# Kernel tuning notes

Hardware: AMD Instinct MI355X
Metric: run time of the kernel (lower is better)

The kernel has to match this reference:

```python
import jax, jax.numpy as jnp
import numpy as np

N_NODES = 100000
N_EDGES = 1600000
N_GRAPHS = 128
DIM = 128
N_LAYERS = 4
EPS = 1e-5


def setup_inputs() -> dict:
    key = jax.random.key(0)
    ks = jax.random.split(key, 8)
    h = jax.random.normal(ks[0], (N_NODES, DIM), dtype=jnp.float32)
    src = jax.random.randint(ks[1], (N_EDGES,), 0, N_NODES, dtype=jnp.int32)
    dst = jax.random.randint(ks[2], (N_EDGES,), 0, N_NODES, dtype=jnp.int32)
    graph_id = jnp.sort(jax.random.randint(ks[3], (N_NODES,), 0, N_GRAPHS, dtype=jnp.int32))
    sc = 1.0 / np.sqrt(DIM)
    W_embed = jax.random.normal(ks[4], (DIM, DIM), dtype=jnp.float32) * sc
    b_embed = jnp.zeros((DIM,), jnp.float32)
    W_layers = jax.random.normal(ks[5], (N_LAYERS, DIM, DIM), dtype=jnp.float32) * sc
    b_layers = jnp.zeros((N_LAYERS, DIM), jnp.float32)
    gamma = jnp.ones((N_LAYERS, DIM), jnp.float32)
    beta = jnp.zeros((N_LAYERS, DIM), jnp.float32)
    return {"h": h, "src": src, "dst": dst, "graph_id": graph_id,
            "W_embed": W_embed, "b_embed": b_embed, "W_layers": W_layers,
            "b_layers": b_layers, "gamma": gamma, "beta": beta}


def _gcn_forward(h, src, dst, graph_id, W_embed, b_embed, W_layers, b_layers, gamma, beta):
    # symmetric GraphConv normalization (norm='both'): D_out^{-1/2} on src, D_in^{-1/2} on dst
    ones_e = jnp.ones((src.shape[0],), h.dtype)
    deg_out = jax.ops.segment_sum(ones_e, src, num_segments=N_NODES)
    deg_in = jax.ops.segment_sum(ones_e, dst, num_segments=N_NODES)
    norm_src = jax.lax.rsqrt(jnp.maximum(deg_out, 1.0))
    norm_dst = jax.lax.rsqrt(jnp.maximum(deg_in, 1.0))

    # input embedding (dropout = identity in eval)
    h = h @ W_embed + b_embed

    for l in range(N_LAYERS):
        h_in = h
        # gather-aggregate-scatter: m_e = h_src * norm_src; sum into dst; scale by norm_dst
        m = (h * norm_src[:, None])[src]                         # [E, D]
        agg = jax.ops.segment_sum(m, dst, num_segments=N_NODES)  # [N, D]
        hl = (agg * norm_dst[:, None]) @ W_layers[l] + b_layers[l]
        # batch norm over node dimension (training-mode batch stats)
        mu = jnp.mean(hl, axis=0)
        var = jnp.var(hl, axis=0)
        hl = (hl - mu) * jax.lax.rsqrt(var + EPS) * gamma[l] + beta[l]
        hl = jax.nn.relu(hl)
        h = hl + h_in  # residual (dims match all layers)

    # mean readout per graph
    sums = jax.ops.segment_sum(h, graph_id, num_segments=N_GRAPHS)           # [G, D]
    cnts = jax.ops.segment_sum(jnp.ones((N_NODES,), h.dtype), graph_id, num_segments=N_GRAPHS)
    return sums / jnp.maximum(cnts, 1.0)[:, None]


def reference(h, src, dst, graph_id, W_embed, b_embed, W_layers, b_layers, gamma, beta):
    return _gcn_forward(h, src, dst, graph_id, W_embed, b_embed, W_layers, b_layers, gamma, beta)
```

## Files before the change

kernel.cpp:

```cpp
#include <hip/hip_runtime.h>
#include <hip/hip_bf16.h>
#include <hip/hip_fp16.h>


#define N_NODES 100000
#define N_EDGES 1600000
#define N_GRAPHS 128
#define DIM 128
#define N_LAYERS 4
#define BN_EPS 1e-5f
#define NBUCK 196
#define EPB 6250
#define SREP 64

typedef __attribute__((ext_vector_type(8))) _Float16 half8;
typedef __attribute__((ext_vector_type(4))) float floatx4;
typedef __attribute__((ext_vector_type(2))) float floatx2;

__global__ __launch_bounds__(256) void binA_k(const int* __restrict__ src,
                                              const int* __restrict__ dst,
                                              int* __restrict__ cnt_d,
                                              int* __restrict__ cnt_s) {
  __shared__ int hd[NBUCK], hs[NBUCK];
  int t = threadIdx.x;
  for (int i = t; i < NBUCK; i += 256) { hd[i] = 0; hs[i] = 0; }
  __syncthreads();
  int e0 = blockIdx.x * EPB;
  for (int e = e0 + t; e < e0 + EPB; e += 256) {
    atomicAdd(&hd[dst[e] >> 9], 1);
    atomicAdd(&hs[src[e] >> 9], 1);
  }
  __syncthreads();
  for (int i = t; i < NBUCK; i += 256) {
    if (hd[i]) atomicAdd(&cnt_d[i], hd[i]);
    if (hs[i]) atomicAdd(&cnt_s[i], hs[i]);
  }
}

__global__ __launch_bounds__(256) void scan196_k(
    const int* __restrict__ cnt_d, const int* __restrict__ cnt_s,
    int* __restrict__ base_d, int* __restrict__ cur_d,
    int* __restrict__ base_s, int* __restrict__ cur_s,
    int* __restrict__ row_start) {
  __shared__ int sd[256], ss[256];
  int t = threadIdx.x;
  int vd = (t < NBUCK) ? cnt_d[t] : 0;
  int vs = (t < NBUCK) ? cnt_s[t] : 0;
  sd[t] = vd;
  ss[t] = vs;
  __syncthreads();
  for (int off = 1; off < 256; off <<= 1) {
    int ad = (t >= off) ? sd[t - off] : 0;
    int as = (t >= off) ? ss[t - off] : 0;
    __syncthreads();
    sd[t] += ad;
    ss[t] += as;
    __syncthreads();
  }
  if (t < NBUCK) {
    base_d[t] = sd[t] - vd;
    cur_d[t] = sd[t] - vd;
    base_s[t] = ss[t] - vs;
    cur_s[t] = ss[t] - vs;
  }
  if (t == 0) {
    base_d[NBUCK] = N_EDGES;
    base_s[NBUCK] = N_EDGES;
    row_start[N_NODES] = N_EDGES;
  }
}

__global__ __launch_bounds__(256) void scat_k(
    const int* __restrict__ src, const int* __restrict__ dst,
    int* __restrict__ cur_d, int* __restrict__ cur_s,
    int* __restrict__ packed, unsigned short* __restrict__ locs) {
  __shared__ int hd[NBUCK], hs[NBUCK];
  int t = threadIdx.x;
  for (int i = t; i < NBUCK; i += 256) { hd[i] = 0; hs[i] = 0; }
  __syncthreads();
  int e0 = blockIdx.x * EPB;
  for (int e = e0 + t; e < e0 + EPB; e += 256) {
    atomicAdd(&hd[dst[e] >> 9], 1);
    atomicAdd(&hs[src[e] >> 9], 1);
  }
  __syncthreads();
  if (t < NBUCK) {
    hd[t] = atomicAdd(&cur_d[t], hd[t]);
    hs[t] = atomicAdd(&cur_s[t], hs[t]);
  }
  __syncthreads();
  for (int e = e0 + t; e < e0 + EPB; e += 256) {
    int s = src[e], d = dst[e];
    int slot = atomicAdd(&hd[d >> 9], 1);
    packed[slot] = ((d & 511) << 17) | s;
    int slot2 = atomicAdd(&hs[s >> 9], 1);
    locs[slot2] = (unsigned short)(s & 511);
  }
}

__global__ __launch_bounds__(256) void cd_k(const int* __restrict__ base_d,
                                            const int* __restrict__ packed,
                                            int* __restrict__ row_start,
                                            int* __restrict__ csr_src) {
  __shared__ int sdeg[512], sinc[512], scur[512];
  int t = threadIdx.x;
  int b = blockIdx.x;
  int nbase = b << 9;
  int e0 = base_d[b], e1 = base_d[b + 1];
  sdeg[t] = 0;
  sdeg[t + 256] = 0;
  __syncthreads();
  for (int e = e0 + t; e < e1; e += 256) atomicAdd(&sdeg[packed[e] >> 17], 1);
  __syncthreads();
  sinc[t] = sdeg[t];
  sinc[t + 256] = sdeg[t + 256];
  __syncthreads();
  for (int off = 1; off < 512; off <<= 1) {
    int a0 = (t >= off) ? sinc[t - off] : 0;
    int i1 = t + 256;
    int a1 = (i1 >= off) ? sinc[i1 - off] : 0;
    __syncthreads();
    sinc[t] += a0;
    sinc[i1] += a1;
    __syncthreads();
  }
#pragma unroll
  for (int half = 0; half < 2; ++half) {
    int j = t + half * 256;
    int lofs = e0 + sinc[j] - sdeg[j];
    scur[j] = lofs;
    int node = nbase + j;
    if (node < N_NODES) row_start[node] = lofs;
  }
  __syncthreads();
  for (int e = e0 + t; e < e1; e += 256) {
    int p = packed[e];
    int slot = atomicAdd(&scur[p >> 17], 1);
    csr_src[slot] = p & 0x1FFFF;
  }
}

__global__ __launch_bounds__(256) void cs_k(const int* __restrict__ base_s,
                                            const unsigned short* __restrict__ locs,
                                            int* __restrict__ deg_out) {
  __shared__ int sdeg[512];
  int t = threadIdx.x;
  int b = blockIdx.x;
  int nbase = b << 9;
  int e0 = base_s[b], e1 = base_s[b + 1];
  sdeg[t] = 0;
  sdeg[t + 256] = 0;
  __syncthreads();
  for (int e = e0 + t; e < e1; e += 256) atomicAdd(&sdeg[locs[e]], 1);
  __syncthreads();
#pragma unroll
  for (int half = 0; half < 2; ++half) {
    int j = t + half * 256;
    int node = nbase + j;
    if (node < N_NODES) deg_out[node] = sdeg[j];
  }
}

__global__ __launch_bounds__(256) void norm_k(const int* __restrict__ deg_out,
                                              const int* __restrict__ row_start,
                                              float* __restrict__ norm_src,
                                              float* __restrict__ norm_dst) {
  int i = blockIdx.x * 256 + threadIdx.x;
  if (i < N_NODES) {
    int din = row_start[i + 1] - row_start[i];
    int dso = deg_out[i] > 1 ? deg_out[i] : 1;
    int dsi = din > 1 ? din : 1;
    norm_src[i] = rsqrtf((float)dso);
    norm_dst[i] = rsqrtf((float)dsi);
  }
}

__global__ __launch_bounds__(256) void wswz_k(const float* __restrict__ W,
                                              __half* __restrict__ Bsw) {
  int w = blockIdx.x >> 3, ct = blockIdx.x & 7;
  int ks = threadIdx.x >> 6, lane = threadIdx.x & 63;
  int n = ct * 16 + (lane & 15);
  int k0 = ks * 32 + (lane >> 4) * 8;
  const float* Wm = W + (size_t)w * 16384;
  __half* o = Bsw + ((((size_t)w * 8 + ct) * 4 + ks) * 64 + lane) * 8;
#pragma unroll
  for (int j = 0; j < 8; ++j) o[j] = __float2half(Wm[(k0 + j) * 128 + n]);
}

__device__ inline void mfma_core16(const __half* sA,
                                   const __half* __restrict__ Bsw,
                                   floatx4 (&acc)[8], int w, int lane,
                                   int quad, int lrow) {
#pragma unroll
  for (int ct = 0; ct < 8; ++ct) acc[ct] = (floatx4)(0.f);
#pragma unroll
  for (int ks = 0; ks < 4; ++ks) {
    int m = w * 16 + lrow;
    half8 afrag = *(const half8*)(&sA[m * 136 + ks * 32 + quad * 8]);
#pragma unroll
    for (int ct = 0; ct < 8; ++ct) {
      half8 bfrag = *(const half8*)(&Bsw[(((size_t)ct * 4 + ks) * 64 + lane) * 8]);
      acc[ct] = __builtin_amdgcn_mfma_f32_16x16x32_f16(afrag, bfrag, acc[ct],
                                                       0, 0, 0);
    }
  }
}

__global__ __launch_bounds__(256) void mfma_gemm_f32in(
    const float* __restrict__ X32, const __half* __restrict__ Bsw,
    const float* __restrict__ bias, __half* __restrict__ A16,
    unsigned char* __restrict__ S8, const float* __restrict__ norm_src) {
  __shared__ __half sA[64 * 136];
  const int tid = threadIdx.x;
  const int w = tid >> 6, lane = tid & 63;
  const int quad = lane >> 4, lrow = lane & 15;
  const int row_base = blockIdx.x * 64;

#pragma unroll
  for (int i = 0; i < 8; ++i) {
    int g = i * 256 + tid;
    int r = g >> 5, q = g & 31;
    int row = row_base + r;
    float4 v = make_float4(0.f, 0.f, 0.f, 0.f);
    if (row < N_NODES) v = ((const float4*)X32)[(size_t)row * 32 + q];
    union { __half2 h[2]; float f[2]; } u;
    u.h[0] = __floats2half2_rn(v.x, v.y);
    u.h[1] = __floats2half2_rn(v.z, v.w);
    *(float2*)(&sA[r * 136 + q * 4]) = *(float2*)u.f;
  }
  __syncthreads();

  floatx4 acc[8];
  mfma_core16(sA, Bsw, acc, w, lane, quad, lrow);

#pragma unroll
  for (int ct = 0; ct < 8; ++ct) {
    int col = ct * 16 + lrow;
    float b = bias[col];
#pragma unroll
    for (int reg = 0; reg < 4; ++reg) {
      int row = row_base + w * 16 + quad * 4 + reg;
      if (row < N_NODES) {
        float y = acc[ct][reg] + b;
        A16[(size_t)row * 128 + col] = __float2half(y);
        unsigned pb =
            __builtin_amdgcn_cvt_pk_fp8_f32(y * norm_src[row], 0.f, 0, false);
        S8[(size_t)row * 128 + col] = (unsigned char)(pb & 0xFF);
      }
    }
  }
}

__global__ __launch_bounds__(256) void mfma_gemm_f16(
    const __half* __restrict__ X16, const __half* __restrict__ Bsw,
    const float* __restrict__ bias, __half* __restrict__ hl16,
    float* __restrict__ stats) {
  __shared__ __half sA[64 * 136];
  const int tid = threadIdx.x;
  const int w = tid >> 6, lane = tid & 63;
  const int quad = lane >> 4, lrow = lane & 15;
  const int row_base = blockIdx.x * 64;

#pragma unroll
  for (int i = 0; i < 4; ++i) {
    int g = i * 256 + tid;
    int r = g >> 4, p = g & 15;
    int row = row_base + r;
    float4 v = make_float4(0.f, 0.f, 0.f, 0.f);
    if (row < N_NODES) v = ((const float4*)X16)[(size_t)row * 16 + p];
    *(float4*)(&sA[r * 136 + p * 8]) = v;
  }
  __syncthreads();

  floatx4 acc[8];
  mfma_core16(sA, Bsw, acc, w, lane, quad, lrow);

  float psum[8], pqsum[8];
#pragma unroll
  for (int ct = 0; ct < 8; ++ct) {
    int col = ct * 16 + lrow;
    float b = bias[col];
    psum[ct] = 0.f;
    pqsum[ct] = 0.f;
#pragma unroll
    for (int reg = 0; reg < 4; ++reg) {
      int row = row_base + w * 16 + quad * 4 + reg;
      if (row < N_NODES) {
        float y = acc[ct][reg] + b;
        hl16[(size_t)row * 128 + col] = __float2half(y);
        psum[ct] += y;
        pqsum[ct] += y * y;
      }
    }
  }

#pragma unroll
  for (int ct = 0; ct < 8; ++ct) {
    psum[ct] += __shfl_xor(psum[ct], 16, 64);
    psum[ct] += __shfl_xor(psum[ct], 32, 64);
    pqsum[ct] += __shfl_xor(pqsum[ct], 16, 64);
    pqsum[ct] += __shfl_xor(pqsum[ct], 32, 64);
  }
  __syncthreads();
  float* sred = (float*)sA;
  if (quad == 0) {
#pragma unroll
    for (int ct = 0; ct < 8; ++ct) {
      sred[w * 128 + ct * 16 + lrow] = psum[ct];
      sred[512 + w * 128 + ct * 16 + lrow] = pqsum[ct];
    }
  }
  __syncthreads();
  if (tid < 128) {
    float s = sred[tid] + sred[128 + tid] + sred[256 + tid] + sred[384 + tid];
    float q = sred[512 + tid] + sred[640 + tid] + sred[768 + tid] +
              sred[896 + tid];
    float* st = stats + (size_t)(blockIdx.x & (SREP - 1)) * 256;
    atomicAdd(&st[tid], s);
    atomicAdd(&st[128 + tid], q);
  }
}

__global__ __launch_bounds__(128) void bn_fin_k(const float* __restrict__ stats,
                                                const float* __restrict__ gamma,
                                                const float* __restrict__ beta,
                                                float* __restrict__ sc_sh) {
  int c = threadIdx.x;
  float s = 0.f, q = 0.f;
  for (int r = 0; r < SREP; ++r) {
    s += stats[r * 256 + c];
    q += stats[r * 256 + 128 + c];
  }
  const float invn = 1.0f / (float)N_NODES;
  float mean = s * invn;
  float var = q * invn - mean * mean;
  var = fmaxf(var, 0.f);
  float sc = gamma[c] * rsqrtf(var + BN_EPS);
  sc_sh[c] = sc;
  sc_sh[128 + c] = beta[c] - mean * sc;
}

__global__ __launch_bounds__(256) void bnrelu_k(
    const __half* __restrict__ hl16, __half* __restrict__ A16,
    unsigned char* __restrict__ S8, const float* __restrict__ sc_sh,
    const float* __restrict__ norm_src, int write_scaled) {
  int idx = blockIdx.x * 256 + threadIdx.x;
  int node = idx >> 4;
  int c8 = idx & 15;
  float4 hv4 = *(const float4*)(hl16 + (size_t)idx * 8);
  float4 av4 = *(const float4*)(A16 + (size_t)idx * 8);
  const __half2* hp = (const __half2*)&hv4;
  const __half2* ap = (const __half2*)&av4;
  const float4* sv = (const float4*)sc_sh;
  float4 s0 = sv[c8 * 2], s1 = sv[c8 * 2 + 1];
  float4 b0 = sv[32 + c8 * 2], b1 = sv[32 + c8 * 2 + 1];
  float n = write_scaled ? norm_src[node] : 0.f;
  float2 f0 = __half22float2(hp[0]), f1 = __half22float2(hp[1]);
  float2 f2 = __half22float2(hp[2]), f3 = __half22float2(hp[3]);
  float2 a0 = __half22float2(ap[0]), a1 = __half22float2(ap[1]);
  float2 a2 = __half22float2(ap[2]), a3 = __half22float2(ap[3]);
  float v[8];
  v[0] = fmaxf(f0.x * s0.x + b0.x, 0.f) + a0.x;
  v[1] = fmaxf(f0.y * s0.y + b0.y, 0.f) + a0.y;
  v[2] = fmaxf(f1.x * s0.z + b0.z, 0.f) + a1.x;
  v[3] = fmaxf(f1.y * s0.w + b0.w, 0.f) + a1.y;
  v[4] = fmaxf(f2.x * s1.x + b1.x, 0.f) + a2.x;
  v[5] = fmaxf(f2.y * s1.y + b1.y, 0.f) + a2.y;
  v[6] = fmaxf(f3.x * s1.z + b1.z, 0.f) + a3.x;
  v[7] = fmaxf(f3.y * s1.w + b1.w, 0.f) + a3.y;
  union { __half2 h[4]; float4 f; } ua;
#pragma unroll
  for (int q = 0; q < 4; ++q)
    ua.h[q] = __floats2half2_rn(v[2 * q], v[2 * q + 1]);
  *(float4*)(A16 + (size_t)idx * 8) = ua.f;
  if (write_scaled) {
    unsigned lo = 0, hi = 0;
    lo = __builtin_amdgcn_cvt_pk_fp8_f32(v[0] * n, v[1] * n, lo, false);
    lo = __builtin_amdgcn_cvt_pk_fp8_f32(v[2] * n, v[3] * n, lo, true);
    hi = __builtin_amdgcn_cvt_pk_fp8_f32(v[4] * n, v[5] * n, hi, false);
    hi = __builtin_amdgcn_cvt_pk_fp8_f32(v[6] * n, v[7] * n, hi, true);
    ((uint2*)S8)[idx] = make_uint2(lo, hi);
  }
}

__device__ inline void accf8(float (&a)[8], uint2 v) {
  floatx2 f;
  f = __builtin_amdgcn_cvt_pk_f32_fp8(v.x, false); a[0] += f.x; a[1] += f.y;
  f = __builtin_amdgcn_cvt_pk_f32_fp8(v.x, true);  a[2] += f.x; a[3] += f.y;
  f = __builtin_amdgcn_cvt_pk_f32_fp8(v.y, false); a[4] += f.x; a[5] += f.y;
  f = __builtin_amdgcn_cvt_pk_f32_fp8(v.y, true);  a[6] += f.x; a[7] += f.y;
}

__global__ __launch_bounds__(256) void gather_k(
    const uint2* __restrict__ Hs, const int* __restrict__ row_start,
    const int* __restrict__ csr_src, const float* __restrict__ norm_dst,
    __half* __restrict__ out) {
  int node = (blockIdx.x * 256 + threadIdx.x) >> 4;
  int lane = threadIdx.x & 15;
  if (node >= N_NODES) return;
  int s0 = row_start[node], s1 = row_start[node + 1];
  float a[8] = {0.f, 0.f, 0.f, 0.f, 0.f, 0.f, 0.f, 0.f};
  for (int e = s0; e < s1; e += 16) {
    int cnt = s1 - e;
    if (cnt > 16) cnt = 16;
    int idx = (lane < cnt) ? csr_src[e + lane] : 0;
    int j = 0;
    for (; j + 8 <= cnt; j += 8) {
      uint2 v0 = Hs[(size_t)__shfl(idx, j, 16) * 16 + lane];
      uint2 v1 = Hs[(size_t)__shfl(idx, j + 1, 16) * 16 + lane];
      uint2 v2 = Hs[(size_t)__shfl(idx, j + 2, 16) * 16 + lane];
      uint2 v3 = Hs[(size_t)__shfl(idx, j + 3, 16) * 16 + lane];
      uint2 v4 = Hs[(size_t)__shfl(idx, j + 4, 16) * 16 + lane];
      uint2 v5 = Hs[(size_t)__shfl(idx, j + 5, 16) * 16 + lane];
      uint2 v6 = Hs[(size_t)__shfl(idx, j + 6, 16) * 16 + lane];
      uint2 v7 = Hs[(size_t)__shfl(idx, j + 7, 16) * 16 + lane];
      accf8(a, v0); accf8(a, v1); accf8(a, v2); accf8(a, v3);
      accf8(a, v4); accf8(a, v5); accf8(a, v6); accf8(a, v7);
    }
    for (; j + 4 <= cnt; j += 4) {
      uint2 v0 = Hs[(size_t)__shfl(idx, j, 16) * 16 + lane];
      uint2 v1 = Hs[(size_t)__shfl(idx, j + 1, 16) * 16 + lane];
      uint2 v2 = Hs[(size_t)__shfl(idx, j + 2, 16) * 16 + lane];
      uint2 v3 = Hs[(size_t)__shfl(idx, j + 3, 16) * 16 + lane];
      accf8(a, v0); accf8(a, v1); accf8(a, v2); accf8(a, v3);
    }
    for (; j < cnt; ++j) {
      accf8(a, Hs[(size_t)__shfl(idx, j, 16) * 16 + lane]);
    }
  }
  float nd = norm_dst[node];
  union { __half2 h[4]; float4 f; } u;
  u.h[0] = __floats2half2_rn(a[0] * nd, a[1] * nd);
  u.h[1] = __floats2half2_rn(a[2] * nd, a[3] * nd);
  u.h[2] = __floats2half2_rn(a[4] * nd, a[5] * nd);
  u.h[3] = __floats2half2_rn(a[6] * nd, a[7] * nd);
  ((float4*)(out + (size_t)node * 128))[lane] = u.f;
}

__global__ __launch_bounds__(256) void gbounds_k(const int* __restrict__ gid,
                                                 int* __restrict__ gstart) {
  int g = threadIdx.x;
  if (g > N_GRAPHS) return;
  int lo = 0, hi = N_NODES;
  while (lo < hi) {
    int mid = (lo + hi) >> 1;
    if (gid[mid] < g) lo = mid + 1; else hi = mid;
  }
  gstart[g] = lo;
}

__global__ __launch_bounds__(128) void gsum_k(const __half* __restrict__ A16,
                                              const int* __restrict__ gid,
                                              float* gsum) {
  int c = threadIdx.x;
  int n0 = blockIdx.x * 128;
  int n1 = n0 + 128;
  if (n1 > N_NODES) n1 = N_NODES;
  int cur = gid[n0];
  float local = 0.f;
  for (int n = n0; n < n1; ++n) {
    int g = gid[n];
    if (g != cur) {
      atomicAdd(&gsum[cur * 128 + c], local);
      local = 0.f;
      cur = g;
    }
    local += __half2float(A16[(size_t)n * 128 + c]);
  }
  atomicAdd(&gsum[cur * 128 + c], local);
}

__global__ __launch_bounds__(128) void gout_k(const float* __restrict__ gsum,
                                              const int* __restrict__ gstart,
                                              float* __restrict__ out) {
  int g = blockIdx.x, c = threadIdx.x;
  float cnt = (float)(gstart[g + 1] - gstart[g]);
  if (cnt < 1.f) cnt = 1.f;
  out[g * 128 + c] = gsum[g * 128 + c] / cnt;
}

extern "C" void kernel_launch(void* const* d_in, const int* in_sizes, int n_in,
                              void* d_out, int out_size, void* d_ws,
                              size_t ws_size, hipStream_t stream) {
  const float* h = (const float*)d_in[0];
  const int* src = (const int*)d_in[1];
  const int* dst = (const int*)d_in[2];
  const int* gid = (const int*)d_in[3];
  const float* W_embed = (const float*)d_in[4];
  const float* b_embed = (const float*)d_in[5];
  const float* W_layers = (const float*)d_in[6];
  const float* b_layers = (const float*)d_in[7];
  const float* gamma = (const float*)d_in[8];
  const float* beta = (const float*)d_in[9];
  float* out = (float*)d_out;
  (void)in_sizes; (void)n_in; (void)out_size; (void)ws_size;

  char* ws = (char*)d_ws;
  size_t o = 0;
  auto alloc = [&](size_t bytes) -> char* {
    char* p = ws + o;
    o = (o + bytes + 255) & ~(size_t)255;
    return p;
  };
  int* cnt_d = (int*)alloc(NBUCK * 4);
  int* cnt_s = (int*)alloc(NBUCK * 4);
  int* base_d = (int*)alloc((NBUCK + 1) * 4);
  int* cur_d = (int*)alloc(NBUCK * 4);
  int* base_s = (int*)alloc((NBUCK + 1) * 4);
  int* cur_s = (int*)alloc(NBUCK * 4);
  float* norm_src = (float*)alloc(N_NODES * 4);
  float* norm_dst = (float*)alloc(N_NODES * 4);
  int* deg_out = (int*)alloc(N_NODES * 4);
  int* row_start = (int*)alloc((N_NODES + 1) * 4);
  int* csr_src = (int*)alloc((size_t)N_EDGES * 4);
  int* packed = (int*)alloc((size_t)N_EDGES * 4);
  unsigned short* locs = (unsigned short*)alloc((size_t)N_EDGES * 2);
  float* stats = (float*)alloc((size_t)SREP * 256 * 4);
  float* gsum = (float*)alloc(N_GRAPHS * 128 * 4);
  int* gstart = (int*)alloc((N_GRAPHS + 1) * 4);
  float* sc_sh = (float*)alloc(256 * 4);
  __half* Bsw = (__half*)alloc(5 * 16384 * 2);
  __half* A16 = (__half*)alloc((size_t)N_NODES * 128 * 2);
  unsigned char* P0f8 = (unsigned char*)alloc((size_t)N_NODES * 128);
  __half* P1h = (__half*)alloc((size_t)N_NODES * 128 * 2);
  __half* H16 = (__half*)alloc((size_t)N_NODES * 128 * 2);

  hipMemsetAsync(cnt_d, 0, 2048, stream);
  hipMemsetAsync(stats, 0, SREP * 256 * 4 + 65536, stream);

  binA_k<<<256, 256, 0, stream>>>(src, dst, cnt_d, cnt_s);
  scan196_k<<<1, 256, 0, stream>>>(cnt_d, cnt_s, base_d, cur_d, base_s, cur_s,
                                   row_start);
  scat_k<<<256, 256, 0, stream>>>(src, dst, cur_d, cur_s, packed, locs);
  cd_k<<<NBUCK, 256, 0, stream>>>(base_d, packed, row_start, csr_src);
  cs_k<<<NBUCK, 256, 0, stream>>>(base_s, locs, deg_out);
  norm_k<<<(N_NODES + 255) / 256, 256, 0, stream>>>(deg_out, row_start,
                                                    norm_src, norm_dst);

  wswz_k<<<8, 256, 0, stream>>>(W_embed, Bsw);
  wswz_k<<<32, 256, 0, stream>>>(W_layers, Bsw + 16384);

  mfma_gemm_f32in<<<(N_NODES + 63) / 64, 256, 0, stream>>>(
      h, Bsw, b_embed, A16, P0f8, norm_src);

  for (int l = 0; l < N_LAYERS; ++l) {
    if (l) hipMemsetAsync(stats, 0, SREP * 256 * 4, stream);
    gather_k<<<(N_NODES * 16 + 255) / 256, 256, 0, stream>>>(
        (const uint2*)P0f8, row_start, csr_src, norm_dst, P1h);
    mfma_gemm_f16<<<(N_NODES + 63) / 64, 256, 0, stream>>>(
        P1h, Bsw + (size_t)(1 + l) * 16384, b_layers + l * DIM, H16, stats);
    bn_fin_k<<<1, 128, 0, stream>>>(stats, gamma + l * DIM, beta + l * DIM,
                                    sc_sh);
    bnrelu_k<<<(N_NODES * 16 + 255) / 256, 256, 0, stream>>>(
        H16, A16, P0f8, sc_sh, norm_src, (l < N_LAYERS - 1) ? 1 : 0);
  }

  gbounds_k<<<1, 256, 0, stream>>>(gid, gstart);
  gsum_k<<<(N_NODES + 127) / 128, 128, 0, stream>>>(A16, gid, gsum);
  gout_k<<<N_GRAPHS, 128, 0, stream>>>(gsum, gstart, out);
}
```

Baseline: 575.0 us.

## Widen gather loads, reuse block histograms, fold norm kernel, batch launches

```diff
diff --git a/kernel.cpp b/kernel.cpp
--- a/kernel.cpp
+++ b/kernel.cpp
@@ -20,7 +20,9 @@
 __global__ __launch_bounds__(256) void binA_k(const int* __restrict__ src,
                                               const int* __restrict__ dst,
                                               int* __restrict__ cnt_d,
-                                              int* __restrict__ cnt_s) {
+                                              int* __restrict__ cnt_s,
+                                              int* __restrict__ bh_d,
+                                              int* __restrict__ bh_s) {
   __shared__ int hd[NBUCK], hs[NBUCK];
   int t = threadIdx.x;
   for (int i = t; i < NBUCK; i += 256) { hd[i] = 0; hs[i] = 0; }
@@ -32,8 +34,11 @@
   }
   __syncthreads();
   for (int i = t; i < NBUCK; i += 256) {
-    if (hd[i]) atomicAdd(&cnt_d[i], hd[i]);
-    if (hs[i]) atomicAdd(&cnt_s[i], hs[i]);
+    int v = hd[i], v2 = hs[i];
+    bh_d[blockIdx.x * NBUCK + i] = v;
+    bh_s[blockIdx.x * NBUCK + i] = v2;
+    if (v) atomicAdd(&cnt_d[i], v);
+    if (v2) atomicAdd(&cnt_s[i], v2);
   }
 }
 
@@ -73,15 +78,13 @@
 __global__ __launch_bounds__(256) void scat_k(
     const int* __restrict__ src, const int* __restrict__ dst,
     int* __restrict__ cur_d, int* __restrict__ cur_s,
+    const int* __restrict__ bh_d, const int* __restrict__ bh_s,
     int* __restrict__ packed, unsigned short* __restrict__ locs) {
   __shared__ int hd[NBUCK], hs[NBUCK];
   int t = threadIdx.x;
-  for (int i = t; i < NBUCK; i += 256) { hd[i] = 0; hs[i] = 0; }
-  __syncthreads();
-  int e0 = blockIdx.x * EPB;
-  for (int e = e0 + t; e < e0 + EPB; e += 256) {
-    atomicAdd(&hd[dst[e] >> 9], 1);
-    atomicAdd(&hs[src[e] >> 9], 1);
+  for (int i = t; i < NBUCK; i += 256) {
+    hd[i] = bh_d[blockIdx.x * NBUCK + i];
+    hs[i] = bh_s[blockIdx.x * NBUCK + i];
   }
   __syncthreads();
   if (t < NBUCK) {
@@ -89,6 +92,7 @@
     hs[t] = atomicAdd(&cur_s[t], hs[t]);
   }
   __syncthreads();
+  int e0 = blockIdx.x * EPB;
   for (int e = e0 + t; e < e0 + EPB; e += 256) {
     int s = src[e], d = dst[e];
     int slot = atomicAdd(&hd[d >> 9], 1);
@@ -101,7 +105,8 @@
 __global__ __launch_bounds__(256) void cd_k(const int* __restrict__ base_d,
                                             const int* __restrict__ packed,
                                             int* __restrict__ row_start,
-                                            int* __restrict__ csr_src) {
+                                            int* __restrict__ csr_src,
+                                            float* __restrict__ norm_dst) {
   __shared__ int sdeg[512], sinc[512], scur[512];
   int t = threadIdx.x;
   int b = blockIdx.x;
@@ -130,7 +135,11 @@
     int lofs = e0 + sinc[j] - sdeg[j];
     scur[j] = lofs;
     int node = nbase + j;
-    if (node < N_NODES) row_start[node] = lofs;
+    if (node < N_NODES) {
+      row_start[node] = lofs;
+      int d = sdeg[j];
+      norm_dst[node] = rsqrtf((float)(d > 1 ? d : 1));
+    }
   }
   __syncthreads();
   for (int e = e0 + t; e < e1; e += 256) {
@@ -142,7 +151,7 @@
 
 __global__ __launch_bounds__(256) void cs_k(const int* __restrict__ base_s,
                                             const unsigned short* __restrict__ locs,
-                                            int* __restrict__ deg_out) {
+                                            float* __restrict__ norm_src) {
   __shared__ int sdeg[512];
   int t = threadIdx.x;
   int b = blockIdx.x;
@@ -157,32 +166,23 @@
   for (int half = 0; half < 2; ++half) {
     int j = t + half * 256;
     int node = nbase + j;
-    if (node < N_NODES) deg_out[node] = sdeg[j];
-  }
-}
-
-__global__ __launch_bounds__(256) void norm_k(const int* __restrict__ deg_out,
-                                              const int* __restrict__ row_start,
-                                              float* __restrict__ norm_src,
-                                              float* __restrict__ norm_dst) {
-  int i = blockIdx.x * 256 + threadIdx.x;
-  if (i < N_NODES) {
-    int din = row_start[i + 1] - row_start[i];
-    int dso = deg_out[i] > 1 ? deg_out[i] : 1;
-    int dsi = din > 1 ? din : 1;
-    norm_src[i] = rsqrtf((float)dso);
-    norm_dst[i] = rsqrtf((float)dsi);
-  }
-}
-
-__global__ __launch_bounds__(256) void wswz_k(const float* __restrict__ W,
+    if (node < N_NODES) {
+      int d = sdeg[j];
+      norm_src[node] = rsqrtf((float)(d > 1 ? d : 1));
+    }
+  }
+}
+
+__global__ __launch_bounds__(256) void wswz_k(const float* __restrict__ W_embed,
+                                              const float* __restrict__ W_layers,
                                               __half* __restrict__ Bsw) {
-  int w = blockIdx.x >> 3, ct = blockIdx.x & 7;
+  int m = blockIdx.x >> 3, ct = blockIdx.x & 7;
+  const float* Wm =
+      (m == 0) ? W_embed : (W_layers + (size_t)(m - 1) * 16384);
   int ks = threadIdx.x >> 6, lane = threadIdx.x & 63;
   int n = ct * 16 + (lane & 15);
   int k0 = ks * 32 + (lane >> 4) * 8;
-  const float* Wm = W + (size_t)w * 16384;
-  __half* o = Bsw + ((((size_t)w * 8 + ct) * 4 + ks) * 64 + lane) * 8;
+  __half* o = Bsw + ((((size_t)m * 8 + ct) * 4 + ks) * 64 + lane) * 8;
 #pragma unroll
   for (int j = 0; j < 8; ++j) o[j] = __float2half(Wm[(k0 + j) * 128 + n]);
 }
@@ -383,58 +383,53 @@
   }
 }
 
-__device__ inline void accf8(float (&a)[8], uint2 v) {
+__device__ inline void accf8x16(float (&a)[16], uint4 v) {
   floatx2 f;
-  f = __builtin_amdgcn_cvt_pk_f32_fp8(v.x, false); a[0] += f.x; a[1] += f.y;
-  f = __builtin_amdgcn_cvt_pk_f32_fp8(v.x, true);  a[2] += f.x; a[3] += f.y;
-  f = __builtin_amdgcn_cvt_pk_f32_fp8(v.y, false); a[4] += f.x; a[5] += f.y;
-  f = __builtin_amdgcn_cvt_pk_f32_fp8(v.y, true);  a[6] += f.x; a[7] += f.y;
+  f = __builtin_amdgcn_cvt_pk_f32_fp8(v.x, false); a[0] += f.x;  a[1] += f.y;
+  f = __builtin_amdgcn_cvt_pk_f32_fp8(v.x, true);  a[2] += f.x;  a[3] += f.y;
+  f = __builtin_amdgcn_cvt_pk_f32_fp8(v.y, false); a[4] += f.x;  a[5] += f.y;
+  f = __builtin_amdgcn_cvt_pk_f32_fp8(v.y, true);  a[6] += f.x;  a[7] += f.y;
+  f = __builtin_amdgcn_cvt_pk_f32_fp8(v.z, false); a[8] += f.x;  a[9] += f.y;
+  f = __builtin_amdgcn_cvt_pk_f32_fp8(v.z, true);  a[10] += f.x; a[11] += f.y;
+  f = __builtin_amdgcn_cvt_pk_f32_fp8(v.w, false); a[12] += f.x; a[13] += f.y;
+  f = __builtin_amdgcn_cvt_pk_f32_fp8(v.w, true);  a[14] += f.x; a[15] += f.y;
 }
 
 __global__ __launch_bounds__(256) void gather_k(
-    const uint2* __restrict__ Hs, const int* __restrict__ row_start,
+    const uint4* __restrict__ Hs, const int* __restrict__ row_start,
     const int* __restrict__ csr_src, const float* __restrict__ norm_dst,
     __half* __restrict__ out) {
-  int node = (blockIdx.x * 256 + threadIdx.x) >> 4;
-  int lane = threadIdx.x & 15;
+  int node = (blockIdx.x * 256 + threadIdx.x) >> 3;
+  int lane = threadIdx.x & 7;
   if (node >= N_NODES) return;
   int s0 = row_start[node], s1 = row_start[node + 1];
-  float a[8] = {0.f, 0.f, 0.f, 0.f, 0.f, 0.f, 0.f, 0.f};
-  for (int e = s0; e < s1; e += 16) {
+  float a[16];
+#pragma unroll
+  for (int i = 0; i < 16; ++i) a[i] = 0.f;
+  for (int e = s0; e < s1; e += 8) {
     int cnt = s1 - e;
-    if (cnt > 16) cnt = 16;
+    if (cnt > 8) cnt = 8;
     int idx = (lane < cnt) ? csr_src[e + lane] : 0;
     int j = 0;
-    for (; j + 8 <= cnt; j += 8) {
-      uint2 v0 = Hs[(size_t)__shfl(idx, j, 16) * 16 + lane];
-      uint2 v1 = Hs[(size_t)__shfl(idx, j + 1, 16) * 16 + lane];
-      uint2 v2 = Hs[(size_t)__shfl(idx, j + 2, 16) * 16 + lane];
-      uint2 v3 = Hs[(size_t)__shfl(idx, j + 3, 16) * 16 + lane];
-      uint2 v4 = Hs[(size_t)__shfl(idx, j + 4, 16) * 16 + lane];
-      uint2 v5 = Hs[(size_t)__shfl(idx, j + 5, 16) * 16 + lane];
-      uint2 v6 = Hs[(size_t)__shfl(idx, j + 6, 16) * 16 + lane];
-      uint2 v7 = Hs[(size_t)__shfl(idx, j + 7, 16) * 16 + lane];
-      accf8(a, v0); accf8(a, v1); accf8(a, v2); accf8(a, v3);
-      accf8(a, v4); accf8(a, v5); accf8(a, v6); accf8(a, v7);
-    }
     for (; j + 4 <= cnt; j += 4) {
-      uint2 v0 = Hs[(size_t)__shfl(idx, j, 16) * 16 + lane];
-      uint2 v1 = Hs[(size_t)__shfl(idx, j + 1, 16) * 16 + lane];
-      uint2 v2 = Hs[(size_t)__shfl(idx, j + 2, 16) * 16 + lane];
-      uint2 v3 = Hs[(size_t)__shfl(idx, j + 3, 16) * 16 + lane];
-      accf8(a, v0); accf8(a, v1); accf8(a, v2); accf8(a, v3);
+      uint4 v0 = Hs[(size_t)__shfl(idx, j, 8) * 8 + lane];
+      uint4 v1 = Hs[(size_t)__shfl(idx, j + 1, 8) * 8 + lane];
+      uint4 v2 = Hs[(size_t)__shfl(idx, j + 2, 8) * 8 + lane];
+      uint4 v3 = Hs[(size_t)__shfl(idx, j + 3, 8) * 8 + lane];
+      accf8x16(a, v0); accf8x16(a, v1); accf8x16(a, v2); accf8x16(a, v3);
     }
     for (; j < cnt; ++j) {
-      accf8(a, Hs[(size_t)__shfl(idx, j, 16) * 16 + lane]);
+      accf8x16(a, Hs[(size_t)__shfl(idx, j, 8) * 8 + lane]);
     }
   }
   float nd = norm_dst[node];
-  union { __half2 h[4]; float4 f; } u;
-  u.h[0] = __floats2half2_rn(a[0] * nd, a[1] * nd);
-  u.h[1] = __floats2half2_rn(a[2] * nd, a[3] * nd);
-  u.h[2] = __floats2half2_rn(a[4] * nd, a[5] * nd);
-  u.h[3] = __floats2half2_rn(a[6] * nd, a[7] * nd);
-  ((float4*)(out + (size_t)node * 128))[lane] = u.f;
+  union { __half2 h[8]; float4 f[2]; } u;
+#pragma unroll
+  for (int q = 0; q < 8; ++q)
+    u.h[q] = __floats2half2_rn(a[2 * q] * nd, a[2 * q + 1] * nd);
+  float4* op = (float4*)(out + (size_t)node * 128 + lane * 16);
+  op[0] = u.f[0];
+  op[1] = u.f[1];
 }
 
 __global__ __launch_bounds__(256) void gbounds_k(const int* __restrict__ gid,
@@ -508,14 +503,15 @@
   int* cur_d = (int*)alloc(NBUCK * 4);
   int* base_s = (int*)alloc((NBUCK + 1) * 4);
   int* cur_s = (int*)alloc(NBUCK * 4);
+  int* bh_d = (int*)alloc((size_t)256 * NBUCK * 4);
+  int* bh_s = (int*)alloc((size_t)256 * NBUCK * 4);
   float* norm_src = (float*)alloc(N_NODES * 4);
   float* norm_dst = (float*)alloc(N_NODES * 4);
-  int* deg_out = (int*)alloc(N_NODES * 4);
   int* row_start = (int*)alloc((N_NODES + 1) * 4);
   int* csr_src = (int*)alloc((size_t)N_EDGES * 4);
   int* packed = (int*)alloc((size_t)N_EDGES * 4);
   unsigned short* locs = (unsigned short*)alloc((size_t)N_EDGES * 2);
-  float* stats = (float*)alloc((size_t)SREP * 256 * 4);
+  float* stats4 = (float*)alloc((size_t)N_LAYERS * SREP * 256 * 4);
   float* gsum = (float*)alloc(N_GRAPHS * 128 * 4);
   int* gstart = (int*)alloc((N_GRAPHS + 1) * 4);
   float* sc_sh = (float*)alloc(256 * 4);
@@ -526,27 +522,26 @@
   __half* H16 = (__half*)alloc((size_t)N_NODES * 128 * 2);
 
   hipMemsetAsync(cnt_d, 0, 2048, stream);
-  hipMemsetAsync(stats, 0, SREP * 256 * 4 + 65536, stream);
-
-  binA_k<<<256, 256, 0, stream>>>(src, dst, cnt_d, cnt_s);
+  hipMemsetAsync(stats4, 0, (size_t)N_LAYERS * SREP * 256 * 4 + 65536, stream);
+
+  binA_k<<<256, 256, 0, stream>>>(src, dst, cnt_d, cnt_s, bh_d, bh_s);
   scan196_k<<<1, 256, 0, stream>>>(cnt_d, cnt_s, base_d, cur_d, base_s, cur_s,
                                    row_start);
-  scat_k<<<256, 256, 0, stream>>>(src, dst, cur_d, cur_s, packed, locs);
-  cd_k<<<NBUCK, 256, 0, stream>>>(base_d, packed, row_start, csr_src);
-  cs_k<<<NBUCK, 256, 0, stream>>>(base_s, locs, deg_out);
-  norm_k<<<(N_NODES + 255) / 256, 256, 0, stream>>>(deg_out, row_start,
-                                                    norm_src, norm_dst);
-
-  wswz_k<<<8, 256, 0, stream>>>(W_embed, Bsw);
-  wswz_k<<<32, 256, 0, stream>>>(W_layers, Bsw + 16384);
+  scat_k<<<256, 256, 0, stream>>>(src, dst, cur_d, cur_s, bh_d, bh_s, packed,
+                                  locs);
+  cd_k<<<NBUCK, 256, 0, stream>>>(base_d, packed, row_start, csr_src,
+                                  norm_dst);
+  cs_k<<<NBUCK, 256, 0, stream>>>(base_s, locs, norm_src);
+
+  wswz_k<<<40, 256, 0, stream>>>(W_embed, W_layers, Bsw);
 
   mfma_gemm_f32in<<<(N_NODES + 63) / 64, 256, 0, stream>>>(
       h, Bsw, b_embed, A16, P0f8, norm_src);
 
   for (int l = 0; l < N_LAYERS; ++l) {
-    if (l) hipMemsetAsync(stats, 0, SREP * 256 * 4, stream);
-    gather_k<<<(N_NODES * 16 + 255) / 256, 256, 0, stream>>>(
-        (const uint2*)P0f8, row_start, csr_src, norm_dst, P1h);
+    float* stats = stats4 + (size_t)l * SREP * 256;
+    gather_k<<<(N_NODES * 8 + 255) / 256, 256, 0, stream>>>(
+        (const uint4*)P0f8, row_start, csr_src, norm_dst, P1h);
     mfma_gemm_f16<<<(N_NODES + 63) / 64, 256, 0, stream>>>(
         P1h, Bsw + (size_t)(1 + l) * 16384, b_layers + l * DIM, H16, stats);
     bn_fin_k<<<1, 128, 0, stream>>>(stats, gamma + l * DIM, beta + l * DIM,
```

Result: no change. 571.6 us (-0.6%).
